# Kernel optimization log

Measured on AMD Instinct MI355X. Metric: run time of the kernel, lower is better.

The kernel has to match this reference:

```python
import jax, jax.numpy as jnp
import numpy as np

B, C, D, H, EXP = 4, 1024, 1024, 16, 4
EPS = 1e-6


def ffn_layernorm(x, w, b):
    # normalize over channel axis (dim 1); w,b have shape (1, C)
    u = jnp.mean(x, axis=1, keepdims=True)
    s = jnp.mean((x - u) ** 2, axis=1, keepdims=True)
    xn = (x - u) / jnp.sqrt(s + EPS)
    return w[:, :, None] * xn + b[:, :, None]


def softmax_one(x):
    # exp(x - max) / (1 + sum exp(x - max)), exactly as the torch SoftmaxOne
    m = jnp.max(x, axis=-1, keepdims=True)
    e = jnp.exp(x - m)
    return e / (1.0 + jnp.sum(e, axis=-1, keepdims=True))


def setup_inputs() -> dict:
    key = jax.random.key(0)
    ks = jax.random.split(key, 20)
    n = lambda k, shape, s=0.02: jax.random.normal(k, shape, dtype=jnp.float32) * s
    inp = {
        "x1": jax.random.normal(ks[0], (B, C, D), dtype=jnp.float32),
        "lnq_w": jnp.ones((1, C), jnp.float32) + n(ks[1], (1, C)),
        "lnq_b": n(ks[2], (1, C)),
        "lnk_w": jnp.ones((1, C), jnp.float32) + n(ks[3], (1, C)),
        "lnk_b": n(ks[4], (1, C)),
        "lnv_w": jnp.ones((1, C), jnp.float32) + n(ks[5], (1, C)),
        "lnv_b": n(ks[6], (1, C)),
        "wq": n(ks[7], (D, D)),
        "bq": n(ks[8], (D,)),
        "wk": n(ks[9], (D, D)),
        "bk": n(ks[10], (D,)),
        "wv": n(ks[11], (D, D)),
        "bv": n(ks[12], (D,)),
        "ffnln_w": jnp.ones((1, C), jnp.float32) + n(ks[13], (1, C)),
        "ffnln_b": n(ks[14], (1, C)),
        "conv1_w": n(ks[15], (C * EXP, C)),
        "conv1_b": n(ks[16], (C * EXP,)),
        "conv2_w": n(ks[17], (C, C * EXP)),
        "conv2_b": n(ks[18], (C,)),
    }
    return inp


def reference(x1, lnq_w, lnq_b, lnk_w, lnk_b, lnv_w, lnv_b,
              wq, bq, wk, bk, wv, bv,
              ffnln_w, ffnln_b, conv1_w, conv1_b, conv2_w, conv2_b):
    b, c, d = x1.shape
    dh = d // H
    q = ffn_layernorm(x1, lnq_w, lnq_b)
    k = ffn_layernorm(x1, lnk_w, lnk_b)
    v = ffn_layernorm(x1, lnv_w, lnv_b)
    # nn.Linear: y = x @ W.T + b, then the torch code's direct reshape
    # (b, c, d) -> (b, H, c, dh) (NOT a transpose-split)
    q = (q @ wq.T + bq).reshape(b, H, c, dh)
    k = (k @ wk.T + bk).reshape(b, H, c, dh)
    v = (v @ wv.T + bv).reshape(b, H, c, dh)
    scale = 1.0 / np.sqrt(dh).astype(np.float32)
    attn = jnp.einsum("bhqe,bhke->bhqk", q * scale, k)
    attn_weights = softmax_one(attn)
    o = jnp.einsum("bhqk,bhke->bhqe", attn_weights, v)
    o = o.transpose(0, 2, 1, 3).reshape(b, c, d)
    x = x1 + o
    # FFN: channel LayerNorm -> 1x1 conv (channel mix) -> GELU -> 1x1 conv
    xl = ffn_layernorm(x, ffnln_w, ffnln_b)
    h1 = jnp.einsum("oc,bcl->bol", conv1_w, xl) + conv1_b[None, :, None]
    h1 = jax.nn.gelu(h1, approximate=False)
    h2 = jnp.einsum("oc,bcl->bol", conv2_w, h1) + conv2_b[None, :, None]
    return (x + h2, attn_weights)
```

## Files before the change

kernel.cpp:

```cpp
#include <hip/hip_runtime.h>
#include <hip/hip_bf16.h>
#include <math.h>


typedef __bf16 bf16;
typedef __bf16 bf16x4 __attribute__((ext_vector_type(4)));
typedef __bf16 bf16x8 __attribute__((ext_vector_type(8)));
typedef float floatx4 __attribute__((ext_vector_type(4)));

#define MFMA16(a, b, c) __builtin_amdgcn_mfma_f32_16x16x32_bf16(a, b, c, 0, 0, 0)

__device__ __forceinline__ void gload16(const void* g, void* l) {
    __builtin_amdgcn_global_load_lds((__attribute__((address_space(1))) void*)g,
                                     (__attribute__((address_space(3))) void*)l,
                                     16, 0, 0);
}

__global__ __launch_bounds__(256)
void cast_all(const float* __restrict__ s0, bf16* __restrict__ d0_,
              const float* __restrict__ s1, bf16* __restrict__ d1_,
              const float* __restrict__ s2, bf16* __restrict__ d2_,
              const float* __restrict__ s3, bf16* __restrict__ d3_,
              const float* __restrict__ s4, bf16* __restrict__ d4_)
{
    int blk = blockIdx.x;
    const float* s; bf16* d; int base;
    if (blk < 1024)      { s = s0; d = d0_; base = blk; }
    else if (blk < 2048) { s = s1; d = d1_; base = blk - 1024; }
    else if (blk < 3072) { s = s2; d = d2_; base = blk - 2048; }
    else if (blk < 7168) { s = s3; d = d3_; base = blk - 3072; }
    else                 { s = s4; d = d4_; base = blk - 7168; }
    long i = ((long)base << 10) + (threadIdx.x << 2);
    float4 v = *(const float4*)(s + i);
    bf16x4 o;
    o[0] = (bf16)v.x; o[1] = (bf16)v.y; o[2] = (bf16)v.z; o[3] = (bf16)v.w;
    *(bf16x4*)(d + i) = o;
}

__global__ __launch_bounds__(256)
void stats_kernel(const float* __restrict__ xin, float* __restrict__ u,
                  float* __restrict__ rstd)
{
    __shared__ float S1[4][64];
    __shared__ float S2[4][64];
    const int b = blockIdx.y;
    const int d0 = blockIdx.x << 6;
    const int tid = threadIdx.x;
    const int dl = tid & 63, cg = tid >> 6;
    const float* xp = xin + ((long)b << 20) + d0 + dl;
    float s = 0.f, sq = 0.f;
    const int cbase = cg << 8;
    for (int c = 0; c < 256; ++c) {
        float v = xp[(long)(cbase + c) << 10];
        s += v; sq += v * v;
    }
    S1[cg][dl] = s; S2[cg][dl] = sq;
    __syncthreads();
    if (tid < 64) {
        float ts = S1[0][tid] + S1[1][tid] + S1[2][tid] + S1[3][tid];
        float tq = S2[0][tid] + S2[1][tid] + S2[2][tid] + S2[3][tid];
        float mu = ts * (1.f / 1024.f);
        float var = tq * (1.f / 1024.f) - mu * mu;
        u[(b << 10) + d0 + tid] = mu;
        rstd[(b << 10) + d0 + tid] = rsqrtf(var + 1e-6f);
    }
}

__global__ __launch_bounds__(256)
void ln_qkv_kernel(const float* __restrict__ x1, const float* __restrict__ u,
                   const float* __restrict__ rs,
                   const float* __restrict__ wq, const float* __restrict__ bq,
                   const float* __restrict__ wk, const float* __restrict__ bk,
                   const float* __restrict__ wv, const float* __restrict__ bv,
                   bf16* __restrict__ lnq, bf16* __restrict__ lnk,
                   bf16* __restrict__ lnv)
{
    const int bc = blockIdx.x;
    const int c = bc & 1023, b = bc >> 10;
    const int d = threadIdx.x << 2;
    const long i = ((long)bc << 10) + d;
    const float4 xv = *(const float4*)(x1 + i);
    const float4 uv = *(const float4*)(u + (b << 10) + d);
    const float4 rv = *(const float4*)(rs + (b << 10) + d);
    float xn0 = (xv.x - uv.x) * rv.x;
    float xn1 = (xv.y - uv.y) * rv.y;
    float xn2 = (xv.z - uv.z) * rv.z;
    float xn3 = (xv.w - uv.w) * rv.w;
    float sw, sb; bf16x4 o;
    sw = wq[c]; sb = bq[c];
    o[0]=(bf16)(sw*xn0+sb); o[1]=(bf16)(sw*xn1+sb); o[2]=(bf16)(sw*xn2+sb); o[3]=(bf16)(sw*xn3+sb);
    *(bf16x4*)(lnq + i) = o;
    sw = wk[c]; sb = bk[c];
    o[0]=(bf16)(sw*xn0+sb); o[1]=(bf16)(sw*xn1+sb); o[2]=(bf16)(sw*xn2+sb); o[3]=(bf16)(sw*xn3+sb);
    *(bf16x4*)(lnk + i) = o;
    sw = wv[c]; sb = bv[c];
    o[0]=(bf16)(sw*xn0+sb); o[1]=(bf16)(sw*xn1+sb); o[2]=(bf16)(sw*xn2+sb); o[3]=(bf16)(sw*xn3+sb);
    *(bf16x4*)(lnv + i) = o;
}

__global__ __launch_bounds__(256)
void gemm_bt(const bf16* __restrict__ Ab, const bf16* __restrict__ Bb,
             void* __restrict__ Outb,
             const float* __restrict__ bias0, const float* __restrict__ bias1,
             const float* __restrict__ bias2, const float* __restrict__ residb,
             long sAz, long sBz, long sOz, long sRz,
             int M, int N, int K, int mode)
{
    __shared__ __align__(16) bf16 As[128 * 32];
    __shared__ __align__(16) bf16 Bs[128 * 32];
    const int z = blockIdx.z;
    const bf16* A = Ab + (long)z * sAz;
    const bf16* B = Bb + (long)z * sBz;
    const float* bias = (z == 0) ? bias0 : (z == 1 ? bias1 : bias2);
    const int m0 = blockIdx.y << 7, n0 = blockIdx.x << 7;
    const int tid = threadIdx.x;
    const int wave = tid >> 6, lane = tid & 63;
    const int wm = (wave & 1) << 6, wn = (wave >> 1) << 6;
    const int lm = lane & 15, lk = (lane >> 4) << 3;
    floatx4 acc[4][4] = {};
    for (int kt = 0; kt < K; kt += 32) {
        const bf16* Ag = A + (long)m0 * K + kt;
        const bf16* Bg = B + (long)n0 * K + kt;
#pragma unroll
        for (int i = 0; i < 2; ++i) {
            int c = tid + (i << 8);
            int row = c >> 2, kc = (c & 3) << 3;
            gload16(Ag + (long)row * K + kc, As + c * 8);
            gload16(Bg + (long)row * K + kc, Bs + c * 8);
        }
        __syncthreads();
        bf16x8 af[4], bfv[4];
#pragma unroll
        for (int mi = 0; mi < 4; ++mi)
            af[mi] = *(const bf16x8*)(As + (wm + mi * 16 + lm) * 32 + lk);
#pragma unroll
        for (int ni = 0; ni < 4; ++ni)
            bfv[ni] = *(const bf16x8*)(Bs + (wn + ni * 16 + lm) * 32 + lk);
#pragma unroll
        for (int mi = 0; mi < 4; ++mi)
#pragma unroll
            for (int ni = 0; ni < 4; ++ni)
                acc[mi][ni] = MFMA16(af[mi], bfv[ni], acc[mi][ni]);
        __syncthreads();
    }
    const int quad = lane >> 4;
    if (mode == 2) {
        float* Out = (float*)Outb + (long)z * sOz;
        const float* R = residb + (long)z * sRz;
#pragma unroll
        for (int mi = 0; mi < 4; ++mi)
#pragma unroll
            for (int ni = 0; ni < 4; ++ni)
#pragma unroll
                for (int r = 0; r < 4; ++r) {
                    int row = m0 + wm + mi * 16 + quad * 4 + r;
                    int col = n0 + wn + ni * 16 + lm;
                    long idx = (long)row * N + col;
                    Out[idx] = acc[mi][ni][r] + bias[row] + R[idx];
                }
    } else {
        bf16* Out = (bf16*)Outb + (long)z * sOz;
#pragma unroll
        for (int mi = 0; mi < 4; ++mi)
#pragma unroll
            for (int ni = 0; ni < 4; ++ni)
#pragma unroll
                for (int r = 0; r < 4; ++r) {
                    int row = m0 + wm + mi * 16 + quad * 4 + r;
                    int col = n0 + wn + ni * 16 + lm;
                    float v = acc[mi][ni][r] + bias[col];
                    if (mode == 1)
                        v = 0.5f * v * (1.0f + erff(v * 0.70710678118654752f));
                    Out[(long)row * N + col] = (bf16)v;
                }
    }
}

__global__ __launch_bounds__(256)
void vtrans_kernel(const bf16* __restrict__ v, bf16* __restrict__ vt)
{
    __shared__ bf16 T[64][66];
    const int p = blockIdx.y;
    const int k0 = blockIdx.x << 6;
    const bf16* V = v + ((long)p << 16);
    bf16* Vt = vt + ((long)p << 16);
    const int tid = threadIdx.x;
    const int e = tid & 63, g = tid >> 6;
#pragma unroll
    for (int j = 0; j < 16; ++j) {
        int kk = (g << 4) + j;
        T[e][kk] = V[((long)(k0 + kk) << 6) + e];
    }
    __syncthreads();
#pragma unroll
    for (int j = 0; j < 16; ++j) {
        int er = (g << 4) + j;
        Vt[((long)er << 10) + k0 + e] = T[er][e];
    }
}

__global__ __launch_bounds__(256)
void attn_kernel(const bf16* __restrict__ q, const bf16* __restrict__ k,
                 const bf16* __restrict__ vt, const float* __restrict__ x1,
                 float* __restrict__ attw, float* __restrict__ x)
{
    __shared__ __align__(16) bf16 Wl[16][1032];
    __shared__ float red[16][4];
    const int s = blockIdx.x;
    const int p = blockIdx.y;
    const int b = p >> 4, h = p & 15;
    const bf16* Qp = q + ((long)b << 20) + ((long)h << 16);
    const bf16* Kp = k + ((long)b << 20) + ((long)h << 16);
    const bf16* Vt = vt + ((long)p << 16);
    const int tid = threadIdx.x, w = tid >> 6, lane = tid & 63;
    const int lm = lane & 15, quad = lane >> 4;
    const int r0 = s << 4, kc0 = w << 8;

    floatx4 acc[16];
#pragma unroll
    for (int t = 0; t < 16; ++t) acc[t] = (floatx4){0.f, 0.f, 0.f, 0.f};

#pragma unroll
    for (int e0 = 0; e0 < 64; e0 += 32) {
        bf16x8 aq = *(const bf16x8*)(Qp + ((long)(r0 + lm) << 6) + e0 + quad * 8);
#pragma unroll
        for (int t = 0; t < 16; ++t) {
            bf16x8 bk = *(const bf16x8*)(Kp + ((long)(kc0 + t * 16 + lm) << 6) + e0 + quad * 8);
            acc[t] = MFMA16(aq, bk, acc[t]);
        }
    }
#pragma unroll
    for (int t = 0; t < 16; ++t)
#pragma unroll
        for (int r = 0; r < 4; ++r) acc[t][r] *= 0.125f;

    float mloc[4];
#pragma unroll
    for (int r = 0; r < 4; ++r) {
        float mm = acc[0][r];
#pragma unroll
        for (int t = 1; t < 16; ++t) mm = fmaxf(mm, acc[t][r]);
        mloc[r] = mm;
    }
#pragma unroll
    for (int off = 1; off < 16; off <<= 1)
#pragma unroll
        for (int r = 0; r < 4; ++r) mloc[r] = fmaxf(mloc[r], __shfl_xor(mloc[r], off, 64));
    if (lm == 0)
#pragma unroll
        for (int r = 0; r < 4; ++r) red[quad * 4 + r][w] = mloc[r];
    __syncthreads();
    float mfin[4];
#pragma unroll
    for (int r = 0; r < 4; ++r) {
        int row = quad * 4 + r;
        mfin[r] = fmaxf(fmaxf(red[row][0], red[row][1]), fmaxf(red[row][2], red[row][3]));
    }
    float sloc[4] = {0.f, 0.f, 0.f, 0.f};
#pragma unroll
    for (int t = 0; t < 16; ++t)
#pragma unroll
        for (int r = 0; r < 4; ++r) {
            float e = __expf(acc[t][r] - mfin[r]);
            acc[t][r] = e;
            sloc[r] += e;
        }
#pragma unroll
    for (int off = 1; off < 16; off <<= 1)
#pragma unroll
        for (int r = 0; r < 4; ++r) sloc[r] += __shfl_xor(sloc[r], off, 64);
    __syncthreads();
    if (lm == 0)
#pragma unroll
        for (int r = 0; r < 4; ++r) red[quad * 4 + r][w] = sloc[r];
    __syncthreads();
    float inv[4];
#pragma unroll
    for (int r = 0; r < 4; ++r) {
        int row = quad * 4 + r;
        inv[r] = 1.f / (1.f + red[row][0] + red[row][1] + red[row][2] + red[row][3]);
    }
    float* attp = attw + ((long)p << 20) + ((long)r0 << 10) + kc0;
#pragma unroll
    for (int r = 0; r < 4; ++r) {
        int row = quad * 4 + r;
        float iv = inv[r];
#pragma unroll
        for (int t = 0; t < 16; ++t) {
            float wv = acc[t][r] * iv;
            attp[((long)row << 10) + t * 16 + lm] = wv;
            Wl[row][kc0 + t * 16 + lm] = (bf16)wv;
        }
    }
    __syncthreads();

    floatx4 opv[4];
#pragma unroll
    for (int ni = 0; ni < 4; ++ni) opv[ni] = (floatx4){0.f, 0.f, 0.f, 0.f};
#pragma unroll
    for (int i = 0; i < 8; ++i) {
        const int kk = kc0 + i * 32;
        bf16x8 a0 = *(const bf16x8*)&Wl[lm][kk + quad * 8];
#pragma unroll
        for (int ni = 0; ni < 4; ++ni) {
            bf16x8 bv = *(const bf16x8*)(Vt + ((long)(ni * 16 + lm) << 10) + kk + quad * 8);
            opv[ni] = MFMA16(a0, bv, opv[ni]);
        }
    }
    __syncthreads();
    float* Ored = (float*)&Wl[0][0];
#pragma unroll
    for (int ni = 0; ni < 4; ++ni)
#pragma unroll
        for (int r = 0; r < 4; ++r)
            Ored[(w * 16 + quad * 4 + r) * 64 + ni * 16 + lm] = opv[ni][r];
    __syncthreads();
    const float* x1p = x1 + ((long)b << 20) + ((long)r0 << 10) + (h << 6);
    float* xp = x + ((long)b << 20) + ((long)r0 << 10) + (h << 6);
#pragma unroll
    for (int j = 0; j < 4; ++j) {
        int el = tid + (j << 8);
        int row = el >> 6, cc = el & 63;
        float o = Ored[row * 64 + cc] + Ored[(16 + row) * 64 + cc]
                + Ored[(32 + row) * 64 + cc] + Ored[(48 + row) * 64 + cc];
        xp[((long)row << 10) + cc] = x1p[((long)row << 10) + cc] + o;
    }
}

__global__ __launch_bounds__(256)
void ln_ffn_t_kernel(const float* __restrict__ x, const float* __restrict__ u2,
                     const float* __restrict__ r2, const float* __restrict__ fw,
                     const float* __restrict__ fb, bf16* __restrict__ xlT)
{
    __shared__ bf16 T[64][66];
    const int b = blockIdx.z;
    const int l0 = blockIdx.x << 6, c0 = blockIdx.y << 6;
    const int tid = threadIdx.x;
    const int ll = tid & 63, g = tid >> 6;
    const float uu = u2[(b << 10) + l0 + ll];
    const float rr = r2[(b << 10) + l0 + ll];
#pragma unroll
    for (int j = 0; j < 16; ++j) {
        int cc = (g << 4) + j;
        float v = x[((long)b << 20) + ((long)(c0 + cc) << 10) + l0 + ll];
        T[ll][cc] = (bf16)(fw[c0 + cc] * (v - uu) * rr + fb[c0 + cc]);
    }
    __syncthreads();
#pragma unroll
    for (int j = 0; j < 16; ++j) {
        int lr = (g << 4) + j;
        xlT[((long)b << 20) + ((long)(l0 + lr) << 10) + c0 + ll] = T[lr][ll];
    }
}

extern "C" void kernel_launch(void* const* d_in, const int* in_sizes, int n_in,
                              void* d_out, int out_size, void* d_ws, size_t ws_size,
                              hipStream_t stream)
{
    const float* x1      = (const float*)d_in[0];
    const float* lnq_w   = (const float*)d_in[1];
    const float* lnq_b   = (const float*)d_in[2];
    const float* lnk_w   = (const float*)d_in[3];
    const float* lnk_b   = (const float*)d_in[4];
    const float* lnv_w   = (const float*)d_in[5];
    const float* lnv_b   = (const float*)d_in[6];
    const float* wq      = (const float*)d_in[7];
    const float* bq      = (const float*)d_in[8];
    const float* wk      = (const float*)d_in[9];
    const float* bk      = (const float*)d_in[10];
    const float* wv      = (const float*)d_in[11];
    const float* bv      = (const float*)d_in[12];
    const float* ffnln_w = (const float*)d_in[13];
    const float* ffnln_b = (const float*)d_in[14];
    const float* conv1_w = (const float*)d_in[15];
    const float* conv1_b = (const float*)d_in[16];
    const float* conv2_w = (const float*)d_in[17];
    const float* conv2_b = (const float*)d_in[18];
    (void)in_sizes; (void)n_in; (void)out_size; (void)ws_size;

    char* ws = (char*)d_ws;
    const size_t OFF_VT   = 65536;
    const size_t OFF_QKV  = OFF_VT  + 8388608;
    const size_t OFF_WQKV = OFF_QKV + 25165824;
    const size_t OFF_X    = OFF_WQKV + 8388608;
    const size_t OFF_W1   = OFF_X   + 16777216;
    const size_t OFF_W2   = OFF_W1  + 8388608;
    float* u1    = (float*)(ws + 0);
    float* rstd1 = (float*)(ws + 16384);
    float* u2    = (float*)(ws + 32768);
    float* r2    = (float*)(ws + 49152);
    bf16*  vt    = (bf16*)(ws + OFF_VT);
    bf16*  qkv   = (bf16*)(ws + OFF_QKV);
    bf16*  wqkvb = (bf16*)(ws + OFF_WQKV);
    float* x     = (float*)(ws + OFF_X);
    bf16*  w1b   = (bf16*)(ws + OFF_W1);
    bf16*  w2b   = (bf16*)(ws + OFF_W2);
    bf16*  h1T   = (bf16*)(ws + OFF_VT);
    bf16*  xlT   = (bf16*)(ws + OFF_WQKV);

    float* out0 = (float*)d_out;
    float* attw = (float*)((char*)d_out + 16777216);
    bf16*  lnqkv = (bf16*)attw;

    cast_all<<<11264, 256, 0, stream>>>(wq, wqkvb, wk, wqkvb + (1 << 20),
                                        wv, wqkvb + (2 << 20), conv1_w, w1b, conv2_w, w2b);
    stats_kernel<<<dim3(16, 4), 256, 0, stream>>>(x1, u1, rstd1);
    ln_qkv_kernel<<<4096, 256, 0, stream>>>(x1, u1, rstd1, lnq_w, lnq_b, lnk_w, lnk_b,
                                            lnv_w, lnv_b, lnqkv, lnqkv + (1L << 22),
                                            lnqkv + (2L << 22));
    gemm_bt<<<dim3(8, 32, 3), 256, 0, stream>>>(lnqkv, wqkvb, qkv, bq, bk, bv, nullptr,
                                                1L << 22, 1L << 20, 1L << 22, 0,
                                                4096, 1024, 1024, 0);
    vtrans_kernel<<<dim3(16, 64), 256, 0, stream>>>(qkv + (2L << 22), vt);
    attn_kernel<<<dim3(64, 64), 256, 0, stream>>>(qkv, qkv + (1L << 22), vt, x1, attw, x);
    stats_kernel<<<dim3(16, 4), 256, 0, stream>>>(x, u2, r2);
    ln_ffn_t_kernel<<<dim3(16, 16, 4), 256, 0, stream>>>(x, u2, r2, ffnln_w, ffnln_b, xlT);
    gemm_bt<<<dim3(32, 8, 4), 256, 0, stream>>>(xlT, w1b, h1T, conv1_b, conv1_b, conv1_b,
                                                nullptr, 1L << 20, 0, 1L << 22, 0,
                                                1024, 4096, 1024, 1);
    gemm_bt<<<dim3(8, 8, 4), 256, 0, stream>>>(w2b, h1T, out0, conv2_b, conv2_b, conv2_b,
                                               x, 0, 1L << 22, 1L << 20, 1L << 20,
                                               1024, 1024, 4096, 2);
}
```

Measured before the change: 753.2 us.

## Split-K the conv2 GEMM, split LN stats, and coalesce attention-weight stores

The channel-statistics reduction is split into four channel chunks with a separate finalize kernel, giving 256 blocks instead of 64. The conv2 GEMM is split along K into two halves: one writes the biased, residual-added output and the other writes partial sums to a scratch buffer, which an extra kernel then adds. This is meant to raise occupancy for these low-parallelism launches. The attention kernel now writes the softmax weights from the LDS bf16 tile using coalesced, nontemporal float4 stores, replacing scattered per-element stores. This means the output weights are bf16-rounded before being widened to float, which costs precision, and the split-K path adds extra memory traffic and two more kernel launches.

```diff
diff --git a/kernel.cpp b/kernel.cpp
--- a/kernel.cpp
+++ b/kernel.cpp
@@ -38,19 +38,19 @@
 }
 
 __global__ __launch_bounds__(256)
-void stats_kernel(const float* __restrict__ xin, float* __restrict__ u,
-                  float* __restrict__ rstd)
+void stats_part(const float* __restrict__ xin, float* __restrict__ ps,
+                float* __restrict__ pq)
 {
     __shared__ float S1[4][64];
     __shared__ float S2[4][64];
-    const int b = blockIdx.y;
+    const int b = blockIdx.z, chunk = blockIdx.y;
     const int d0 = blockIdx.x << 6;
     const int tid = threadIdx.x;
     const int dl = tid & 63, cg = tid >> 6;
     const float* xp = xin + ((long)b << 20) + d0 + dl;
+    const int cbase = (chunk << 8) + (cg << 6);
     float s = 0.f, sq = 0.f;
-    const int cbase = cg << 8;
-    for (int c = 0; c < 256; ++c) {
+    for (int c = 0; c < 64; ++c) {
         float v = xp[(long)(cbase + c) << 10];
         s += v; sq += v * v;
     }
@@ -59,11 +59,24 @@
     if (tid < 64) {
         float ts = S1[0][tid] + S1[1][tid] + S1[2][tid] + S1[3][tid];
         float tq = S2[0][tid] + S2[1][tid] + S2[2][tid] + S2[3][tid];
-        float mu = ts * (1.f / 1024.f);
-        float var = tq * (1.f / 1024.f) - mu * mu;
-        u[(b << 10) + d0 + tid] = mu;
-        rstd[(b << 10) + d0 + tid] = rsqrtf(var + 1e-6f);
-    }
+        int idx = ((b * 4 + chunk) << 10) + d0 + tid;
+        ps[idx] = ts; pq[idx] = tq;
+    }
+}
+
+__global__ __launch_bounds__(256)
+void stats_fin(const float* __restrict__ ps, const float* __restrict__ pq,
+               float* __restrict__ u, float* __restrict__ rstd)
+{
+    int i = (blockIdx.x << 8) + threadIdx.x;
+    int b = i >> 10, d = i & 1023;
+    int base = (b << 12) + d;
+    float s = ps[base] + ps[base + 1024] + ps[base + 2048] + ps[base + 3072];
+    float q = pq[base] + pq[base + 1024] + pq[base + 2048] + pq[base + 3072];
+    float mu = s * (1.f / 1024.f);
+    float var = q * (1.f / 1024.f) - mu * mu;
+    u[i] = mu;
+    rstd[i] = rsqrtf(var + 1e-6f);
 }
 
 __global__ __launch_bounds__(256)
@@ -100,25 +113,26 @@
 
 __global__ __launch_bounds__(256)
 void gemm_bt(const bf16* __restrict__ Ab, const bf16* __restrict__ Bb,
-             void* __restrict__ Outb,
+             void* __restrict__ Outb, float* __restrict__ Part,
              const float* __restrict__ bias0, const float* __restrict__ bias1,
              const float* __restrict__ bias2, const float* __restrict__ residb,
-             long sAz, long sBz, long sOz, long sRz,
-             int M, int N, int K, int mode)
+             long sAz, long sBz, long sOz, long sRz, long sPz,
+             int M, int N, int K, int Ksub, int zdiv, int mode)
 {
     __shared__ __align__(16) bf16 As[128 * 32];
     __shared__ __align__(16) bf16 Bs[128 * 32];
     const int z = blockIdx.z;
-    const bf16* A = Ab + (long)z * sAz;
-    const bf16* B = Bb + (long)z * sBz;
-    const float* bias = (z == 0) ? bias0 : (z == 1 ? bias1 : bias2);
+    const int zb = z / zdiv, kz = z % zdiv;
+    const bf16* A = Ab + (long)zb * sAz + (long)kz * Ksub;
+    const bf16* B = Bb + (long)zb * sBz + (long)kz * Ksub;
+    const float* bias = (zb == 0) ? bias0 : (zb == 1 ? bias1 : bias2);
     const int m0 = blockIdx.y << 7, n0 = blockIdx.x << 7;
     const int tid = threadIdx.x;
     const int wave = tid >> 6, lane = tid & 63;
     const int wm = (wave & 1) << 6, wn = (wave >> 1) << 6;
     const int lm = lane & 15, lk = (lane >> 4) << 3;
     floatx4 acc[4][4] = {};
-    for (int kt = 0; kt < K; kt += 32) {
+    for (int kt = 0; kt < Ksub; kt += 32) {
         const bf16* Ag = A + (long)m0 * K + kt;
         const bf16* Bg = B + (long)n0 * K + kt;
 #pragma unroll
@@ -145,21 +159,35 @@
     }
     const int quad = lane >> 4;
     if (mode == 2) {
-        float* Out = (float*)Outb + (long)z * sOz;
-        const float* R = residb + (long)z * sRz;
-#pragma unroll
-        for (int mi = 0; mi < 4; ++mi)
-#pragma unroll
-            for (int ni = 0; ni < 4; ++ni)
-#pragma unroll
-                for (int r = 0; r < 4; ++r) {
-                    int row = m0 + wm + mi * 16 + quad * 4 + r;
-                    int col = n0 + wn + ni * 16 + lm;
-                    long idx = (long)row * N + col;
-                    Out[idx] = acc[mi][ni][r] + bias[row] + R[idx];
-                }
+        if (kz == 0) {
+            float* Out = (float*)Outb + (long)zb * sOz;
+            const float* R = residb + (long)zb * sRz;
+#pragma unroll
+            for (int mi = 0; mi < 4; ++mi)
+#pragma unroll
+                for (int ni = 0; ni < 4; ++ni)
+#pragma unroll
+                    for (int r = 0; r < 4; ++r) {
+                        int row = m0 + wm + mi * 16 + quad * 4 + r;
+                        int col = n0 + wn + ni * 16 + lm;
+                        long idx = (long)row * N + col;
+                        Out[idx] = acc[mi][ni][r] + bias[row] + R[idx];
+                    }
+        } else {
+            float* Out = Part + (long)zb * sPz;
+#pragma unroll
+            for (int mi = 0; mi < 4; ++mi)
+#pragma unroll
+                for (int ni = 0; ni < 4; ++ni)
+#pragma unroll
+                    for (int r = 0; r < 4; ++r) {
+                        int row = m0 + wm + mi * 16 + quad * 4 + r;
+                        int col = n0 + wn + ni * 16 + lm;
+                        Out[(long)row * N + col] = acc[mi][ni][r];
+                    }
+        }
     } else {
-        bf16* Out = (bf16*)Outb + (long)z * sOz;
+        bf16* Out = (bf16*)Outb + (long)zb * sOz;
 #pragma unroll
         for (int mi = 0; mi < 4; ++mi)
 #pragma unroll
@@ -174,6 +202,16 @@
                     Out[(long)row * N + col] = (bf16)v;
                 }
     }
+}
+
+__global__ __launch_bounds__(256)
+void addpart(float* __restrict__ out, const float* __restrict__ part)
+{
+    long i = (((long)blockIdx.x << 8) + threadIdx.x) << 2;
+    float4 o = *(const float4*)(out + i);
+    float4 p = *(const float4*)(part + i);
+    o.x += p.x; o.y += p.y; o.z += p.z; o.w += p.w;
+    *(float4*)(out + i) = o;
 }
 
 __global__ __launch_bounds__(256)
@@ -280,17 +318,13 @@
         int row = quad * 4 + r;
         inv[r] = 1.f / (1.f + red[row][0] + red[row][1] + red[row][2] + red[row][3]);
     }
-    float* attp = attw + ((long)p << 20) + ((long)r0 << 10) + kc0;
 #pragma unroll
     for (int r = 0; r < 4; ++r) {
         int row = quad * 4 + r;
         float iv = inv[r];
 #pragma unroll
-        for (int t = 0; t < 16; ++t) {
-            float wv = acc[t][r] * iv;
-            attp[((long)row << 10) + t * 16 + lm] = wv;
-            Wl[row][kc0 + t * 16 + lm] = (bf16)wv;
-        }
+        for (int t = 0; t < 16; ++t)
+            Wl[row][kc0 + t * 16 + lm] = (bf16)(acc[t][r] * iv);
     }
     __syncthreads();
 
@@ -305,6 +339,17 @@
         for (int ni = 0; ni < 4; ++ni) {
             bf16x8 bv = *(const bf16x8*)(Vt + ((long)(ni * 16 + lm) << 10) + kk + quad * 8);
             opv[ni] = MFMA16(a0, bv, opv[ni]);
+        }
+    }
+    {
+        float* attp = attw + ((long)p << 20) + ((long)r0 << 10);
+#pragma unroll
+        for (int i = 0; i < 16; ++i) {
+            int v4 = (i << 8) + tid;
+            int row = v4 >> 8, col = (v4 & 255) << 2;
+            bf16x4 wv = *(const bf16x4*)&Wl[row][col];
+            floatx4 o = {(float)wv[0], (float)wv[1], (float)wv[2], (float)wv[3]};
+            __builtin_nontemporal_store(o, (floatx4*)(attp + ((long)row << 10) + col));
         }
     }
     __syncthreads();
@@ -379,24 +424,27 @@
     (void)in_sizes; (void)n_in; (void)out_size; (void)ws_size;
 
     char* ws = (char*)d_ws;
-    const size_t OFF_VT   = 65536;
-    const size_t OFF_QKV  = OFF_VT  + 8388608;
-    const size_t OFF_WQKV = OFF_QKV + 25165824;
-    const size_t OFF_X    = OFF_WQKV + 8388608;
-    const size_t OFF_W1   = OFF_X   + 16777216;
-    const size_t OFF_W2   = OFF_W1  + 8388608;
+    const size_t OFF_VT   = 262144;
+    const size_t OFF_QKV  = OFF_VT   + 8388608;
+    const size_t OFF_WQKV = OFF_QKV  + 25165824;
+    const size_t OFF_W1   = OFF_WQKV + 8388608;
+    const size_t OFF_X    = OFF_W1   + 8388608;
+    const size_t OFF_W2   = OFF_X    + 16777216;
     float* u1    = (float*)(ws + 0);
-    float* rstd1 = (float*)(ws + 16384);
+    float* r1    = (float*)(ws + 16384);
     float* u2    = (float*)(ws + 32768);
     float* r2    = (float*)(ws + 49152);
+    float* ps    = (float*)(ws + 65536);
+    float* pq    = (float*)(ws + 131072);
     bf16*  vt    = (bf16*)(ws + OFF_VT);
     bf16*  qkv   = (bf16*)(ws + OFF_QKV);
     bf16*  wqkvb = (bf16*)(ws + OFF_WQKV);
+    bf16*  w1b   = (bf16*)(ws + OFF_W1);
     float* x     = (float*)(ws + OFF_X);
-    bf16*  w1b   = (bf16*)(ws + OFF_W1);
     bf16*  w2b   = (bf16*)(ws + OFF_W2);
     bf16*  h1T   = (bf16*)(ws + OFF_VT);
     bf16*  xlT   = (bf16*)(ws + OFF_WQKV);
+    float* part  = (float*)(ws + OFF_WQKV);
 
     float* out0 = (float*)d_out;
     float* attw = (float*)((char*)d_out + 16777216);
@@ -404,21 +452,24 @@
 
     cast_all<<<11264, 256, 0, stream>>>(wq, wqkvb, wk, wqkvb + (1 << 20),
                                         wv, wqkvb + (2 << 20), conv1_w, w1b, conv2_w, w2b);
-    stats_kernel<<<dim3(16, 4), 256, 0, stream>>>(x1, u1, rstd1);
-    ln_qkv_kernel<<<4096, 256, 0, stream>>>(x1, u1, rstd1, lnq_w, lnq_b, lnk_w, lnk_b,
+    stats_part<<<dim3(16, 4, 4), 256, 0, stream>>>(x1, ps, pq);
+    stats_fin<<<16, 256, 0, stream>>>(ps, pq, u1, r1);
+    ln_qkv_kernel<<<4096, 256, 0, stream>>>(x1, u1, r1, lnq_w, lnq_b, lnk_w, lnk_b,
                                             lnv_w, lnv_b, lnqkv, lnqkv + (1L << 22),
                                             lnqkv + (2L << 22));
-    gemm_bt<<<dim3(8, 32, 3), 256, 0, stream>>>(lnqkv, wqkvb, qkv, bq, bk, bv, nullptr,
-                                                1L << 22, 1L << 20, 1L << 22, 0,
-                                                4096, 1024, 1024, 0);
+    gemm_bt<<<dim3(8, 32, 3), 256, 0, stream>>>(lnqkv, wqkvb, qkv, nullptr, bq, bk, bv,
+                                                nullptr, 1L << 22, 1L << 20, 1L << 22, 0, 0,
+                                                4096, 1024, 1024, 1024, 1, 0);
     vtrans_kernel<<<dim3(16, 64), 256, 0, stream>>>(qkv + (2L << 22), vt);
     attn_kernel<<<dim3(64, 64), 256, 0, stream>>>(qkv, qkv + (1L << 22), vt, x1, attw, x);
-    stats_kernel<<<dim3(16, 4), 256, 0, stream>>>(x, u2, r2);
+    stats_part<<<dim3(16, 4, 4), 256, 0, stream>>>(x, ps, pq);
+    stats_fin<<<16, 256, 0, stream>>>(ps, pq, u2, r2);
     ln_ffn_t_kernel<<<dim3(16, 16, 4), 256, 0, stream>>>(x, u2, r2, ffnln_w, ffnln_b, xlT);
-    gemm_bt<<<dim3(32, 8, 4), 256, 0, stream>>>(xlT, w1b, h1T, conv1_b, conv1_b, conv1_b,
-                                                nullptr, 1L << 20, 0, 1L << 22, 0,
-                                                1024, 4096, 1024, 1);
-    gemm_bt<<<dim3(8, 8, 4), 256, 0, stream>>>(w2b, h1T, out0, conv2_b, conv2_b, conv2_b,
-                                               x, 0, 1L << 22, 1L << 20, 1L << 20,
-                                               1024, 1024, 4096, 2);
-}
+    gemm_bt<<<dim3(32, 8, 4), 256, 0, stream>>>(xlT, w1b, h1T, nullptr, conv1_b, conv1_b,
+                                                conv1_b, nullptr, 1L << 20, 0, 1L << 22, 0, 0,
+                                                1024, 4096, 1024, 1024, 1, 1);
+    gemm_bt<<<dim3(8, 8, 8), 256, 0, stream>>>(w2b, h1T, out0, part, conv2_b, conv2_b,
+                                               conv2_b, x, 0, 1L << 22, 1L << 20, 1L << 20,
+                                               1L << 20, 1024, 1024, 4096, 2048, 2, 2);
+    addpart<<<4096, 256, 0, stream>>>(out0, part);
+}
```

After: 677.2 us. -10.1%, faster.
